# Performance work log

Hardware: AMD Instinct MI355X
Metric: run time of the kernel (lower is better)

The kernel has to match this reference:

```python
import jax, jax.numpy as jnp
import numpy as np

B, L, D = 32, 256, 1024
H = 8
DQ = D // H            # 128, dim_q == dim_k
DS = 64                # dim_s
DM = 256               # dim_mlp_s
DF = 4096              # dim_feedforward
EPS = 1e-5


def _layernorm(x, g, b):
    mu = jnp.mean(x, axis=-1, keepdims=True)
    var = jnp.mean(jnp.square(x - mu), axis=-1, keepdims=True)
    return (x - mu) * jax.lax.rsqrt(var + EPS) * g + b


def setup_inputs() -> dict:
    key = jax.random.key(0)
    ks = jax.random.split(key, 20)
    s = 0.02
    inp = {
        'src': jax.random.normal(ks[0], (B, L, D), jnp.float32),
        'sf': jax.random.normal(ks[1], (B, DS), jnp.float32),
        'atten_mask': jax.random.randint(ks[2], (B, L, L), 0, 2, jnp.int32),
        # per-head projections, stacked over heads (in,out layout)
        'qw': jax.random.normal(ks[3], (H, D, DQ), jnp.float32) * s,
        'qb': jnp.zeros((H, DQ), jnp.float32),
        'kw': jax.random.normal(ks[4], (H, D, DQ), jnp.float32) * s,
        'kb': jnp.zeros((H, DQ), jnp.float32),
        'vw': jax.random.normal(ks[5], (H, D, DQ), jnp.float32) * s,
        'vb': jnp.zeros((H, DQ), jnp.float32),
        # per-head bias MLP: dim_s -> dim_mlp_s -> L*L
        'b1w': jax.random.normal(ks[6], (H, DS, DM), jnp.float32) * s,
        'b1b': jnp.zeros((H, DM), jnp.float32),
        'b2w': jax.random.normal(ks[7], (H, DM, L * L), jnp.float32) * s,
        'b2b': jnp.zeros((H, L * L), jnp.float32),
        # output projection
        'ow': jax.random.normal(ks[8], (H * DQ, D), jnp.float32) * s,
        'ob': jnp.zeros((D,), jnp.float32),
        # layernorms
        'ln1_g': jnp.ones((D,), jnp.float32), 'ln1_b': jnp.zeros((D,), jnp.float32),
        'ln2_g': jnp.ones((D,), jnp.float32), 'ln2_b': jnp.zeros((D,), jnp.float32),
        # feed-forward
        'w1': jax.random.normal(ks[9], (D, DF), jnp.float32) * s,
        'bf1': jnp.zeros((DF,), jnp.float32),
        'w2': jax.random.normal(ks[10], (DF, D), jnp.float32) * s,
        'bf2': jnp.zeros((D,), jnp.float32),
    }
    return inp


def reference(src, sf, atten_mask, qw, qb, kw, kb, vw, vb, b1w, b1b, b2w, b2b,
              ow, ob, ln1_g, ln1_b, ln2_g, ln2_b, w1, bf1, w2, bf2):
    mask = atten_mask.astype(bool)                      # (B,L,L)
    # per-head projections: (H,B,L,DQ)
    q = jnp.einsum('bld,hdq->hblq', src, qw) + qb[:, None, None, :]
    k = jnp.einsum('bld,hdq->hblq', src, kw) + kb[:, None, None, :]
    v = jnp.einsum('bld,hdq->hblq', src, vw) + vb[:, None, None, :]
    scale = q.shape[-1] ** 0.5
    scores = jnp.einsum('hblq,hbmq->hblm', q, k) / scale
    # masked_fill with constant 1e-9 (NOT -inf), as in the original
    scores = jnp.where(mask[None], jnp.float32(1e-9), scores)
    # per-head learned bias from side features, added AFTER softmax
    hid = jax.nn.relu(jnp.einsum('bs,hsm->hbm', sf, b1w) + b1b[:, None, :])
    bias = (jnp.einsum('hbm,hmn->hbn', hid, b2w) + b2b[:, None, :]).reshape(H, B, L, L)
    soft = jax.nn.softmax(scores, axis=-1) + bias
    out = jnp.einsum('hblm,hbmv->hblv', soft, v)        # (H,B,L,DQ)
    # faithful to original: each head's result is indexed [0] -> batch element 0
    head0 = out[:, 0]                                   # (H,L,DQ)
    hidden = jnp.transpose(head0, (1, 0, 2)).reshape(L, H * DQ)
    attn = hidden @ ow + ob                             # (L,D), broadcasts over batch
    x = _layernorm(src + attn[None], ln1_g, ln1_b)      # (B,L,D)
    ffn = jax.nn.relu(x @ w1 + bf1) @ w2 + bf2
    return _layernorm(x + ffn, ln2_g, ln2_b)
```

## Files before the change

kernel.cpp:

```cpp
#include <hip/hip_runtime.h>

typedef unsigned short u16;
typedef short s16x8 __attribute__((ext_vector_type(8)));
typedef u16 u16x4 __attribute__((ext_vector_type(4)));
typedef float f32x4 __attribute__((ext_vector_type(4)));

#define B_ 32
#define L_ 256
#define D_ 1024
#define H_ 8
#define DQ_ 128
#define DS_ 64
#define DM_ 256
#define DF_ 4096

__device__ __forceinline__ u16 f2bf(float f) {
  unsigned u = __float_as_uint(f);
  unsigned r = (u + 0x7FFFu + ((u >> 16) & 1u)) >> 16;
  return (u16)r;
}
__device__ __forceinline__ float bf2f(u16 x) {
  return __uint_as_float(((unsigned)x) << 16);
}

__device__ __forceinline__ f32x4 mfma16(s16x8 a, s16x8 b, f32x4 c) {
  return __builtin_amdgcn_mfma_f32_16x16x32_bf16(a, b, c, 0, 0, 0);
}

#define GLDS16(g, l)                                                        \
  __builtin_amdgcn_global_load_lds(                                         \
      (__attribute__((address_space(1))) const void*)(g),                   \
      (__attribute__((address_space(3))) void*)(l), 16, 0, 0)

__device__ __forceinline__ void tile_tr(const float* __restrict__ ip,
                                        u16* __restrict__ op, int K, int N,
                                        int bx, int by, float (*t)[33], int tid) {
  const int tx = tid & 31, ty = tid >> 5;
  const long n0 = (long)bx * 32, k0 = (long)by * 32;
#pragma unroll
  for (int i = 0; i < 4; ++i)
    t[ty + i * 8][tx] = ip[(k0 + ty + i * 8) * (long)N + n0 + tx];
  __syncthreads();
#pragma unroll
  for (int i = 0; i < 4; ++i)
    op[(n0 + ty + i * 8) * (long)K + k0 + tx] = f2bf(t[tx][ty + i * 8]);
}

__global__ __launch_bounds__(256) void prep(
    const float* __restrict__ qw, const float* __restrict__ kw,
    const float* __restrict__ vw, const float* __restrict__ ow,
    const float* __restrict__ w1, const float* __restrict__ w2,
    const float* __restrict__ src, const float* __restrict__ sf,
    const float* __restrict__ b1w, const float* __restrict__ b1b,
    u16* __restrict__ qwT, u16* __restrict__ kwT, u16* __restrict__ vwT,
    u16* __restrict__ owT, u16* __restrict__ w1T, u16* __restrict__ w2T,
    u16* __restrict__ src0b, float* __restrict__ nzv, int* __restrict__ nzi,
    int* __restrict__ nzcnt) {
  const int b = blockIdx.x;
  const int tid = threadIdx.x;
  __shared__ float t[32][33];
  __shared__ float s_sf[DS_];
  __shared__ int wcnt[4];
  if (b < 3072) {
    const int z = b >> 7, rem = b & 127;
    const int sel = z >> 3, h = z & 7;
    const float* ip = (sel == 0 ? qw : (sel == 1 ? kw : vw)) + (long)h * D_ * DQ_;
    u16* op = (sel == 0 ? qwT : (sel == 1 ? kwT : vwT)) + (long)h * DQ_ * D_;
    tile_tr(ip, op, D_, DQ_, rem & 3, rem >> 2, t, tid);
  } else if (b < 4096) {
    const int rem = b - 3072;
    tile_tr(ow, owT, D_, D_, rem & 31, rem >> 5, t, tid);
  } else if (b < 8192) {
    const int rem = b - 4096;
    tile_tr(w1, w1T, D_, DF_, rem & 127, rem >> 7, t, tid);
  } else if (b < 12288) {
    const int rem = b - 8192;
    tile_tr(w2, w2T, DF_, D_, rem & 31, rem >> 5, t, tid);
  } else if (b < 12544) {
    const int rem = b - 12288;
    const int i = (rem * 256 + tid) * 4;
    float4 v = *(const float4*)(src + i);
    u16x4 o = {f2bf(v.x), f2bf(v.y), f2bf(v.z), f2bf(v.w)};
    *(u16x4*)(src0b + i) = o;
  } else {
    const int h = b - 12544;
    if (tid < DS_) s_sf[tid] = sf[tid];
    __syncthreads();
    float a = b1b[h * DM_ + tid];
    const float* wp = b1w + (long)h * DS_ * DM_ + tid;
#pragma unroll 8
    for (int s = 0; s < DS_; ++s) a += s_sf[s] * wp[s * DM_];
    a = fmaxf(a, 0.f);
    const unsigned long long bal = __ballot(a > 0.f);
    const int lane = tid & 63, wv = tid >> 6;
    const int pc = __popcll(bal);
    if (lane == 0) wcnt[wv] = pc;
    __syncthreads();
    int base = 0;
    for (int i = 0; i < wv; ++i) base += wcnt[i];
    const int pos = base + __popcll(bal & ((1ull << lane) - 1ull));
    if (a > 0.f) { nzv[h * DM_ + pos] = a; nzi[h * DM_ + pos] = tid; }
    if (tid == 255) nzcnt[h] = base + pc;
  }
}

__global__ __launch_bounds__(256) void phase2(
    const float* __restrict__ nzv, const int* __restrict__ nzi,
    const int* __restrict__ nzcnt, const float* __restrict__ b2w,
    const float* __restrict__ b2b, float* __restrict__ biasb,
    const u16* __restrict__ src0b, const u16* __restrict__ qwT,
    const u16* __restrict__ kwT, const u16* __restrict__ vwT,
    const float* __restrict__ qb, const float* __restrict__ kb,
    const float* __restrict__ vb, u16* __restrict__ q0, u16* __restrict__ k0,
    u16* __restrict__ v0T) {
  const int b = blockIdx.x;
  const int tid = threadIdx.x;
  __shared__ float sv[DM_];
  __shared__ int si[DM_];
  __shared__ u16 smA[128 * 32];
  __shared__ u16 smB[128 * 32];
  if (b < 512) {
    const int h = b >> 6;
    const int n0 = (b & 63) << 10;
    const int nnz = nzcnt[h];
    if (tid < DM_) { sv[tid] = nzv[h * DM_ + tid]; si[tid] = nzi[h * DM_ + tid]; }
    __syncthreads();
    const float* wb = b2w + (long)h * DM_ * 65536 + n0 + tid * 4;
    float4 acc = {0.f, 0.f, 0.f, 0.f};
    int j = 0;
    for (; j + 4 <= nnz; j += 4) {
      const float4 a0 = *(const float4*)(wb + (long)si[j] * 65536);
      const float4 a1 = *(const float4*)(wb + (long)si[j + 1] * 65536);
      const float4 a2 = *(const float4*)(wb + (long)si[j + 2] * 65536);
      const float4 a3 = *(const float4*)(wb + (long)si[j + 3] * 65536);
      const float v0 = sv[j], v1 = sv[j + 1], v2 = sv[j + 2], v3 = sv[j + 3];
      acc.x += v0 * a0.x + v1 * a1.x + v2 * a2.x + v3 * a3.x;
      acc.y += v0 * a0.y + v1 * a1.y + v2 * a2.y + v3 * a3.y;
      acc.z += v0 * a0.z + v1 * a1.z + v2 * a2.z + v3 * a3.z;
      acc.w += v0 * a0.w + v1 * a1.w + v2 * a2.w + v3 * a3.w;
    }
    for (; j < nnz; ++j) {
      const float4 a0 = *(const float4*)(wb + (long)si[j] * 65536);
      const float v0 = sv[j];
      acc.x += v0 * a0.x; acc.y += v0 * a0.y; acc.z += v0 * a0.z; acc.w += v0 * a0.w;
    }
    const float4 bb = *(const float4*)(b2b + (long)h * 65536 + n0 + tid * 4);
    float4 o = {acc.x + bb.x, acc.y + bb.y, acc.z + bb.z, acc.w + bb.w};
    *(float4*)(biasb + (long)h * 65536 + n0 + tid * 4) = o;
  } else {
    const int r = b - 512;
    const int z = r >> 1, sel = z >> 3, h = z & 7;
    const long tm = (long)(r & 1) * 128;
    const int K = D_;
    const u16* BT = (sel == 0 ? qwT : (sel == 1 ? kwT : vwT)) + (long)h * DQ_ * D_;
    const float* bias = (sel == 0 ? qb : (sel == 1 ? kb : vb)) + h * DQ_;
    const int lane = tid & 63;
    const int wv = tid >> 6;
    const int wr = wv >> 1, wc = wv & 1;
    const u16* ga = src0b + (tm + (tid >> 2)) * (long)K + (tid & 3) * 8;
    const u16* gb = BT + (long)(tid >> 2) * K + (tid & 3) * 8;
    const long rstep = 64L * K;
    u16* la = &smA[tid * 8];
    u16* lb = &smB[tid * 8];
    f32x4 acc[4][4];
#pragma unroll
    for (int m = 0; m < 4; ++m)
#pragma unroll
      for (int n = 0; n < 4; ++n) acc[m][n] = (f32x4){0.f, 0.f, 0.f, 0.f};
    for (int k0_ = 0; k0_ < K; k0_ += 32) {
      GLDS16(ga + k0_, la);
      GLDS16(ga + rstep + k0_, la + 64 * 32);
      GLDS16(gb + k0_, lb);
      GLDS16(gb + rstep + k0_, lb + 64 * 32);
      __syncthreads();
      s16x8 af[4], bf[4];
      const int ka = (lane >> 4) * 8;
      const int ra = wr * 64 + (lane & 15);
      const int rb = wc * 64 + (lane & 15);
#pragma unroll
      for (int m = 0; m < 4; ++m) af[m] = *(const s16x8*)&smA[(ra + m * 16) * 32 + ka];
#pragma unroll
      for (int n = 0; n < 4; ++n) bf[n] = *(const s16x8*)&smB[(rb + n * 16) * 32 + ka];
#pragma unroll
      for (int m = 0; m < 4; ++m)
#pragma unroll
        for (int n = 0; n < 4; ++n) acc[m][n] = mfma16(af[m], bf[n], acc[m][n]);
      __syncthreads();
    }
    const long crow0 = tm + wr * 64 + ((lane >> 4) * 4);
    const long ccol0 = wc * 64 + (lane & 15);
#pragma unroll
    for (int m = 0; m < 4; ++m) {
#pragma unroll
      for (int n = 0; n < 4; ++n) {
#pragma unroll
        for (int i = 0; i < 4; ++i) {
          const long row = crow0 + m * 16 + i;
          const long col = ccol0 + n * 16;
          const float v = acc[m][n][i] + bias[col];
          if (sel < 2) {
            u16* o = (sel == 0 ? q0 : k0) + (long)h * L_ * DQ_;
            o[row * DQ_ + col] = f2bf(v);
          } else {
            v0T[(long)h * DQ_ * L_ + col * L_ + row] = f2bf(v);
          }
        }
      }
    }
  }
}

__global__ __launch_bounds__(256) void gemm_bt(
    const u16* __restrict__ A, const u16* __restrict__ BT, float* __restrict__ C,
    const float* __restrict__ bias, int K, int ldc) {
  __shared__ u16 smA[128 * 32];
  __shared__ u16 smB[128 * 32];
  const int tid = threadIdx.x;
  const int lane = tid & 63;
  const int wv = tid >> 6;
  const int wr = wv >> 1, wc = wv & 1;
  const long tm = (long)blockIdx.x * 128;
  const long tn = (long)blockIdx.y * 128;

  const u16* ga = A + (tm + (tid >> 2)) * (long)K + (tid & 3) * 8;
  const u16* gb = BT + (tn + (tid >> 2)) * (long)K + (tid & 3) * 8;
  const long rstep = 64L * K;
  u16* la = &smA[tid * 8];
  u16* lb = &smB[tid * 8];

  f32x4 acc[4][4];
#pragma unroll
  for (int m = 0; m < 4; ++m)
#pragma unroll
    for (int n = 0; n < 4; ++n) acc[m][n] = (f32x4){0.f, 0.f, 0.f, 0.f};

  for (int k0 = 0; k0 < K; k0 += 32) {
    GLDS16(ga + k0, la);
    GLDS16(ga + rstep + k0, la + 64 * 32);
    GLDS16(gb + k0, lb);
    GLDS16(gb + rstep + k0, lb + 64 * 32);
    __syncthreads();
    s16x8 af[4], bf[4];
    const int ka = (lane >> 4) * 8;
    const int ra = wr * 64 + (lane & 15);
    const int rb = wc * 64 + (lane & 15);
#pragma unroll
    for (int m = 0; m < 4; ++m) af[m] = *(const s16x8*)&smA[(ra + m * 16) * 32 + ka];
#pragma unroll
    for (int n = 0; n < 4; ++n) bf[n] = *(const s16x8*)&smB[(rb + n * 16) * 32 + ka];
#pragma unroll
    for (int m = 0; m < 4; ++m)
#pragma unroll
      for (int n = 0; n < 4; ++n) acc[m][n] = mfma16(af[m], bf[n], acc[m][n]);
    __syncthreads();
  }

  const long crow0 = tm + wr * 64 + ((lane >> 4) * 4);
  const long ccol0 = tn + wc * 64 + (lane & 15);
#pragma unroll
  for (int m = 0; m < 4; ++m)
#pragma unroll
    for (int n = 0; n < 4; ++n)
#pragma unroll
      for (int i = 0; i < 4; ++i) {
        const long row = crow0 + m * 16 + i;
        const long col = ccol0 + n * 16;
        C[row * (long)ldc + col] = acc[m][n][i] + bias[col];
      }
}

template <int BN, int EPI>
__global__ __launch_bounds__(512, 2) void gemm8p(
    const u16* __restrict__ A, const u16* __restrict__ BT, void* __restrict__ Cv,
    const float* __restrict__ bias, const void* __restrict__ R, int M, int N,
    int K, int ldc) {
  extern __shared__ char lds[];
  constexpr int NR = BN / 64;
  constexpr int NHB = BN / 128;
  constexpr int BUF = 32768 + BN * 128;
  constexpr int WST = (NHB == 2) ? 4 : 2;
  const int tid = threadIdx.x;
  const int lane = tid & 63;
  const int w = tid >> 6;
  const int wr = w >> 2, wc = w & 3;

  const int total = gridDim.x;
  int bid = blockIdx.x;
  int s = ((total & 7) == 0) ? ((bid & 7) * (total >> 3) + (bid >> 3)) : bid;
  const int gn = N / BN;
  const long tm = (long)(s / gn) * 256;
  const long tn = (long)(s % gn) * BN;
  const int NT = K >> 6;

  auto stageA = [&](int half, int t) {
    char* hb = lds + (long)(t & 1) * BUF + half * 16384;
    const u16* g = A + (tm + half * 128) * (long)K + (long)t * 64;
#pragma unroll
    for (int j = 0; j < 2; ++j) {
      const int idx = j * 512 + tid;
      const int r = idx >> 3;
      const int c16 = (idx & 7) ^ (r & 7);
      GLDS16(g + (long)r * K + c16 * 8, hb + idx * 16);
    }
  };
  auto stageB = [&](int half, int t) {
    char* hb = lds + (long)(t & 1) * BUF + 32768 + half * 16384;
    const u16* g = BT + (tn + half * 128) * (long)K + (long)t * 64;
#pragma unroll
    for (int j = 0; j < 2; ++j) {
      const int idx = j * 512 + tid;
      const int r = idx >> 3;
      const int c16 = (idx & 7) ^ (r & 7);
      GLDS16(g + (long)r * K + c16 * 8, hb + idx * 16);
    }
  };

  stageA(0, 0);
  stageA(1, 0);
  stageB(0, 0);
  if (NHB == 2) stageB(1, 0);
  stageB(0, 1);
  if (NHB == 2) stageB(1, 1);
  asm volatile("s_waitcnt vmcnt(%0)" ::"n"(WST) : "memory");
  __builtin_amdgcn_s_barrier();

  f32x4 acc[8][NR];
#pragma unroll
  for (int m = 0; m < 8; ++m)
#pragma unroll
    for (int n = 0; n < NR; ++n) acc[m][n] = (f32x4){0.f, 0.f, 0.f, 0.f};

  const int lk = (lane >> 4) * 16;
  const int lr = lane & 15;

  for (int t = 0; t < NT; ++t) {
    const char* bp = lds + (long)(t & 1) * BUF;
    s16x8 bfr[NR][2];
#pragma unroll
    for (int p = 0; p < 4; ++p) {
      if (p == 0) {
#pragma unroll
        for (int ni = 0; ni < NR; ++ni) {
          const int brow = wc * (BN / 4) + ni * 16 + lr;
#pragma unroll
          for (int ks = 0; ks < 2; ++ks) {
            const int kb = (ks * 64 + lk) ^ ((brow & 7) << 4);
            bfr[ni][ks] = *(const s16x8*)(bp + 32768 + brow * 128 + kb);
          }
        }
      }
      s16x8 afr[2][2];
#pragma unroll
      for (int rI = 0; rI < 2; ++rI) {
        const int arow = wr * 128 + (2 * p + rI) * 16 + lr;
#pragma unroll
        for (int ks = 0; ks < 2; ++ks) {
          const int kb = (ks * 64 + lk) ^ ((arow & 7) << 4);
          afr[rI][ks] = *(const s16x8*)(bp + arow * 128 + kb);
        }
      }
      if (p == 0) {
        if (t + 1 < NT) stageA(0, t + 1);
      } else if (p == 1) {
        if (t + 1 < NT) stageA(1, t + 1);
      } else if (p == 2) {
        if (t + 2 < NT) stageB(0, t + 2);
      } else {
        if (NHB == 2 && t + 2 < NT) stageB(1, t + 2);
      }
      __builtin_amdgcn_s_barrier();
      __builtin_amdgcn_s_setprio(1);
#pragma unroll
      for (int rI = 0; rI < 2; ++rI)
#pragma unroll
        for (int ni = 0; ni < NR; ++ni)
#pragma unroll
          for (int ks = 0; ks < 2; ++ks)
            acc[2 * p + rI][ni] = mfma16(afr[rI][ks], bfr[ni][ks], acc[2 * p + rI][ni]);
      __builtin_amdgcn_s_setprio(0);
      if (p == 3) {
        if (t + 2 < NT) {
          asm volatile("s_waitcnt vmcnt(%0)" ::"n"(WST) : "memory");
        } else if (t + 1 < NT) {
          asm volatile("s_waitcnt vmcnt(0)" ::: "memory");
        }
      }
      __builtin_amdgcn_s_barrier();
    }
  }

  const long crow0 = tm + wr * 128 + ((lane >> 4) * 4);
  const long ccol0 = tn + wc * (BN / 4) + lr;
#pragma unroll
  for (int m = 0; m < 8; ++m) {
#pragma unroll
    for (int n = 0; n < NR; ++n) {
#pragma unroll
      for (int i = 0; i < 4; ++i) {
        const long row = crow0 + m * 16 + i;
        const long col = ccol0 + n * 16;
        const float v = acc[m][n][i] + bias[col];
        if constexpr (EPI == 1) {
          ((u16*)Cv)[row * (long)ldc + col] = f2bf(fmaxf(v, 0.f));
        } else {
          const float r = bf2f(((const u16*)R)[row * (long)ldc + col]);
          ((u16*)Cv)[row * (long)ldc + col] = f2bf(v + r);
        }
      }
    }
  }
}

__global__ __launch_bounds__(64) void attn_kernel(
    const u16* __restrict__ q0, const u16* __restrict__ k0,
    const u16* __restrict__ vT, const float* __restrict__ biasb,
    const int* __restrict__ mask0, u16* __restrict__ hidden) {
  const int lane = threadIdx.x;
  const int h = blockIdx.y;
  const int r0 = blockIdx.x * 16;
  const u16* q = q0 + (long)h * L_ * DQ_;
  const u16* k = k0 + (long)h * L_ * DQ_;
  const u16* v = vT + (long)h * DQ_ * L_;
  const int lg = lane >> 4;
  const int ll = lane & 15;

  s16x8 aq[4];
#pragma unroll
  for (int kk = 0; kk < 4; ++kk)
    aq[kk] = *(const s16x8*)(q + (long)(r0 + ll) * DQ_ + kk * 32 + lg * 8);

  float sc[16][4];
  const float scale = 0.08838834764831845f;
#pragma unroll
  for (int t = 0; t < 16; ++t) {
    f32x4 a = {0.f, 0.f, 0.f, 0.f};
#pragma unroll
    for (int kk = 0; kk < 4; ++kk) {
      s16x8 bf = *(const s16x8*)(k + (long)(t * 16 + ll) * DQ_ + kk * 32 + lg * 8);
      a = mfma16(aq[kk], bf, a);
    }
#pragma unroll
    for (int i = 0; i < 4; ++i) {
      const int row = r0 + lg * 4 + i;
      const int col = t * 16 + ll;
      float s = a[i] * scale;
      if (mask0[row * L_ + col] != 0) s = 1e-9f;
      sc[t][i] = s;
    }
  }
#pragma unroll
  for (int i = 0; i < 4; ++i) {
    float mx = sc[0][i];
#pragma unroll
    for (int t = 1; t < 16; ++t) mx = fmaxf(mx, sc[t][i]);
#pragma unroll
    for (int d = 1; d < 16; d <<= 1) mx = fmaxf(mx, __shfl_xor(mx, d));
    float sum = 0.f;
#pragma unroll
    for (int t = 0; t < 16; ++t) {
      const float e = __expf(sc[t][i] - mx);
      sc[t][i] = e;
      sum += e;
    }
#pragma unroll
    for (int d = 1; d < 16; d <<= 1) sum += __shfl_xor(sum, d);
    const float inv = 1.f / sum;
    const int row = r0 + lg * 4 + i;
#pragma unroll
    for (int t = 0; t < 16; ++t)
      sc[t][i] = sc[t][i] * inv + biasb[(long)h * 65536 + (long)row * 256 + t * 16 + ll];
  }
  __shared__ float sm[16 * 256];
#pragma unroll
  for (int t = 0; t < 16; ++t)
#pragma unroll
    for (int i = 0; i < 4; ++i)
      sm[(lg * 4 + i) * 256 + t * 16 + ll] = sc[t][i];
  __syncthreads();
  s16x8 af[8];
#pragma unroll
  for (int kk = 0; kk < 8; ++kk) {
    const float* ap = &sm[ll * 256 + kk * 32 + lg * 8];
    s16x8 t8;
#pragma unroll
    for (int j = 0; j < 8; ++j) t8[j] = (short)f2bf(ap[j]);
    af[kk] = t8;
  }
#pragma unroll
  for (int n = 0; n < 8; ++n) {
    f32x4 a = {0.f, 0.f, 0.f, 0.f};
#pragma unroll
    for (int kk = 0; kk < 8; ++kk) {
      s16x8 bf = *(const s16x8*)(v + (long)(n * 16 + ll) * 256 + kk * 32 + lg * 8);
      a = mfma16(af[kk], bf, a);
    }
#pragma unroll
    for (int i = 0; i < 4; ++i) {
      const int row = r0 + lg * 4 + i;
      const int col = n * 16 + ll;
      hidden[(long)row * 1024 + h * 128 + col] = f2bf(a[i]);
    }
  }
}

template <int MODE>
__global__ __launch_bounds__(256) void ln_kernel(
    const void* __restrict__ in0v, const float* __restrict__ add1,
    const float* __restrict__ g, const float* __restrict__ bb,
    void* __restrict__ outv) {
  const int tid = threadIdx.x;
  const long row = blockIdx.x;
  float4 v;
  if constexpr (MODE == 0) {
    v = ((const float4*)((const float*)in0v + row * D_))[tid];
    const float4 u = ((const float4*)(add1 + (row & (L_ - 1)) * D_))[tid];
    v.x += u.x; v.y += u.y; v.z += u.z; v.w += u.w;
  } else {
    const uint2 pk = *(const uint2*)((const u16*)in0v + row * D_ + tid * 4);
    v.x = __uint_as_float((pk.x & 0xFFFFu) << 16);
    v.y = __uint_as_float(pk.x & 0xFFFF0000u);
    v.z = __uint_as_float((pk.y & 0xFFFFu) << 16);
    v.w = __uint_as_float(pk.y & 0xFFFF0000u);
  }
  float s = v.x + v.y + v.z + v.w;
  float q = v.x * v.x + v.y * v.y + v.z * v.z + v.w * v.w;
#pragma unroll
  for (int d = 1; d < 64; d <<= 1) { s += __shfl_xor(s, d); q += __shfl_xor(q, d); }
  __shared__ float ss[4], sq[4];
  const int wv = tid >> 6;
  if ((tid & 63) == 0) { ss[wv] = s; sq[wv] = q; }
  __syncthreads();
  s = ss[0] + ss[1] + ss[2] + ss[3];
  q = sq[0] + sq[1] + sq[2] + sq[3];
  const float mu = s * (1.f / D_);
  const float var = q * (1.f / D_) - mu * mu;
  const float rs = rsqrtf(var + 1e-5f);
  const float4 gv = ((const float4*)g)[tid];
  const float4 bv = ((const float4*)bb)[tid];
  float4 o;
  o.x = (v.x - mu) * rs * gv.x + bv.x;
  o.y = (v.y - mu) * rs * gv.y + bv.y;
  o.z = (v.z - mu) * rs * gv.z + bv.z;
  o.w = (v.w - mu) * rs * gv.w + bv.w;
  if constexpr (MODE == 0) {
    uint2 pk;
    pk.x = (unsigned)f2bf(o.x) | ((unsigned)f2bf(o.y) << 16);
    pk.y = (unsigned)f2bf(o.z) | ((unsigned)f2bf(o.w) << 16);
    *(uint2*)((u16*)outv + row * D_ + tid * 4) = pk;
  } else {
    ((float4*)((float*)outv + row * D_))[tid] = o;
  }
}

extern "C" void kernel_launch(void* const* d_in, const int* in_sizes, int n_in,
                              void* d_out, int out_size, void* d_ws, size_t ws_size,
                              hipStream_t stream) {
  (void)in_sizes; (void)n_in; (void)out_size; (void)ws_size;
  const float* src = (const float*)d_in[0];
  const float* sf = (const float*)d_in[1];
  const int* mask = (const int*)d_in[2];
  const float* qw = (const float*)d_in[3];
  const float* qb = (const float*)d_in[4];
  const float* kw = (const float*)d_in[5];
  const float* kb = (const float*)d_in[6];
  const float* vw = (const float*)d_in[7];
  const float* vb = (const float*)d_in[8];
  const float* b1w = (const float*)d_in[9];
  const float* b1b = (const float*)d_in[10];
  const float* b2w = (const float*)d_in[11];
  const float* b2b = (const float*)d_in[12];
  const float* ow = (const float*)d_in[13];
  const float* ob = (const float*)d_in[14];
  const float* ln1g = (const float*)d_in[15];
  const float* ln1b = (const float*)d_in[16];
  const float* ln2g = (const float*)d_in[17];
  const float* ln2b = (const float*)d_in[18];
  const float* w1 = (const float*)d_in[19];
  const float* bf1 = (const float*)d_in[20];
  const float* w2 = (const float*)d_in[21];
  const float* bf2 = (const float*)d_in[22];
  float* out = (float*)d_out;

  char* ws = (char*)d_ws;
  size_t off = 0;
  auto alloc = [&](size_t bytes) {
    void* p = ws + off;
    off += (bytes + 255) & ~(size_t)255;
    return p;
  };
  u16* qwT = (u16*)alloc((size_t)H_ * DQ_ * D_ * 2);
  u16* kwT = (u16*)alloc((size_t)H_ * DQ_ * D_ * 2);
  u16* vwT = (u16*)alloc((size_t)H_ * DQ_ * D_ * 2);
  u16* owT = (u16*)alloc((size_t)D_ * D_ * 2);
  u16* w1T = (u16*)alloc((size_t)DF_ * D_ * 2);
  u16* w2T = (u16*)alloc((size_t)D_ * DF_ * 2);
  u16* src0b = (u16*)alloc((size_t)L_ * D_ * 2);
  u16* q0 = (u16*)alloc((size_t)H_ * L_ * DQ_ * 2);
  u16* k0 = (u16*)alloc((size_t)H_ * L_ * DQ_ * 2);
  u16* v0T = (u16*)alloc((size_t)H_ * DQ_ * L_ * 2);
  float* nzv = (float*)alloc((size_t)H_ * DM_ * 4);
  int* nzi = (int*)alloc((size_t)H_ * DM_ * 4);
  int* nzcnt = (int*)alloc(256);
  float* biasb = (float*)alloc((size_t)H_ * L_ * L_ * 4);
  u16* hidden = (u16*)alloc((size_t)L_ * H_ * DQ_ * 2);
  float* attnvec = (float*)alloc((size_t)L_ * D_ * 4);
  u16* xb = (u16*)alloc((size_t)B_ * L_ * D_ * 2);
  u16* ffnh = (u16*)alloc((size_t)B_ * L_ * DF_ * 2);
  u16* yb = (u16*)alloc((size_t)B_ * L_ * D_ * 2);

  hipFuncSetAttribute((const void*)gemm8p<256, 1>,
                      hipFuncAttributeMaxDynamicSharedMemorySize, 131072);
  hipFuncSetAttribute((const void*)gemm8p<128, 2>,
                      hipFuncAttributeMaxDynamicSharedMemorySize, 98304);

  const dim3 b256(256);
  prep<<<dim3(12552), b256, 0, stream>>>(qw, kw, vw, ow, w1, w2, src, sf, b1w, b1b,
                                         qwT, kwT, vwT, owT, w1T, w2T, src0b, nzv,
                                         nzi, nzcnt);
  phase2<<<dim3(560), b256, 0, stream>>>(nzv, nzi, nzcnt, b2w, b2b, biasb, src0b,
                                         qwT, kwT, vwT, qb, kb, vb, q0, k0, v0T);
  attn_kernel<<<dim3(16, H_), dim3(64), 0, stream>>>(q0, k0, v0T, biasb, mask, hidden);
  gemm_bt<<<dim3(2, 8), b256, 0, stream>>>(hidden, owT, attnvec, ob, D_, D_);
  ln_kernel<0><<<dim3(B_ * L_), b256, 0, stream>>>(src, attnvec, ln1g, ln1b, xb);
  gemm8p<256, 1><<<dim3(512), dim3(512), 131072, stream>>>(
      xb, w1T, ffnh, bf1, nullptr, B_ * L_, DF_, D_, DF_);
  gemm8p<128, 2><<<dim3(256), dim3(512), 98304, stream>>>(
      ffnh, w2T, yb, bf2, xb, B_ * L_, D_, DF_, D_);
  ln_kernel<1><<<dim3(B_ * L_), b256, 0, stream>>>(yb, nullptr, ln2g, ln2b, out);
}
```

Measured before the change: 329.0 us.

## Rebalance prep kernels and split attention into softmax·V plus bias·V GEMM

Moves the large weight transposes (ow, w1, w2) out of the first prep kernel into the same launch as the QKV projection GEMM, so the small QKV GEMM blocks overlap with transpose work. The bias-MLP second layer now runs concurrently with the attention softmax·V computation in one launch, storing the bias in bf16. Because the bias is added after softmax, (softmax+bias)·V is decomposed into softmax·V plus a separate bias·V tiled GEMM that accumulates into hidden. The aim is to remove serial launch tails and the fp32 bias traffic. The cost is an extra kernel, a read-modify-write of hidden, and extra bf16 rounding of the bias and of the partial sums.

```diff
diff --git a/kernel.cpp b/kernel.cpp
--- a/kernel.cpp
+++ b/kernel.cpp
@@ -46,16 +46,13 @@
     op[(n0 + ty + i * 8) * (long)K + k0 + tx] = f2bf(t[tx][ty + i * 8]);
 }
 
-__global__ __launch_bounds__(256) void prep(
+__global__ __launch_bounds__(256) void prep1(
     const float* __restrict__ qw, const float* __restrict__ kw,
-    const float* __restrict__ vw, const float* __restrict__ ow,
-    const float* __restrict__ w1, const float* __restrict__ w2,
-    const float* __restrict__ src, const float* __restrict__ sf,
-    const float* __restrict__ b1w, const float* __restrict__ b1b,
-    u16* __restrict__ qwT, u16* __restrict__ kwT, u16* __restrict__ vwT,
-    u16* __restrict__ owT, u16* __restrict__ w1T, u16* __restrict__ w2T,
-    u16* __restrict__ src0b, float* __restrict__ nzv, int* __restrict__ nzi,
-    int* __restrict__ nzcnt) {
+    const float* __restrict__ vw, const float* __restrict__ src,
+    const float* __restrict__ sf, const float* __restrict__ b1w,
+    const float* __restrict__ b1b, u16* __restrict__ qwT, u16* __restrict__ kwT,
+    u16* __restrict__ vwT, u16* __restrict__ src0b, float* __restrict__ nzv,
+    int* __restrict__ nzi, int* __restrict__ nzcnt) {
   const int b = blockIdx.x;
   const int tid = threadIdx.x;
   __shared__ float t[32][33];
@@ -67,23 +64,14 @@
     const float* ip = (sel == 0 ? qw : (sel == 1 ? kw : vw)) + (long)h * D_ * DQ_;
     u16* op = (sel == 0 ? qwT : (sel == 1 ? kwT : vwT)) + (long)h * DQ_ * D_;
     tile_tr(ip, op, D_, DQ_, rem & 3, rem >> 2, t, tid);
-  } else if (b < 4096) {
+  } else if (b < 3328) {
     const int rem = b - 3072;
-    tile_tr(ow, owT, D_, D_, rem & 31, rem >> 5, t, tid);
-  } else if (b < 8192) {
-    const int rem = b - 4096;
-    tile_tr(w1, w1T, D_, DF_, rem & 127, rem >> 7, t, tid);
-  } else if (b < 12288) {
-    const int rem = b - 8192;
-    tile_tr(w2, w2T, DF_, D_, rem & 31, rem >> 5, t, tid);
-  } else if (b < 12544) {
-    const int rem = b - 12288;
     const int i = (rem * 256 + tid) * 4;
     float4 v = *(const float4*)(src + i);
     u16x4 o = {f2bf(v.x), f2bf(v.y), f2bf(v.z), f2bf(v.w)};
     *(u16x4*)(src0b + i) = o;
   } else {
-    const int h = b - 12544;
+    const int h = b - 3328;
     if (tid < DS_) s_sf[tid] = sf[tid];
     __syncthreads();
     float a = b1b[h * DM_ + tid];
@@ -104,22 +92,102 @@
   }
 }
 
-__global__ __launch_bounds__(256) void phase2(
-    const float* __restrict__ nzv, const int* __restrict__ nzi,
-    const int* __restrict__ nzcnt, const float* __restrict__ b2w,
-    const float* __restrict__ b2b, float* __restrict__ biasb,
+__global__ __launch_bounds__(256) void prep2(
     const u16* __restrict__ src0b, const u16* __restrict__ qwT,
     const u16* __restrict__ kwT, const u16* __restrict__ vwT,
     const float* __restrict__ qb, const float* __restrict__ kb,
     const float* __restrict__ vb, u16* __restrict__ q0, u16* __restrict__ k0,
-    u16* __restrict__ v0T) {
+    u16* __restrict__ v0T, const float* __restrict__ ow,
+    const float* __restrict__ w1, const float* __restrict__ w2,
+    u16* __restrict__ owT, u16* __restrict__ w1T, u16* __restrict__ w2T) {
   const int b = blockIdx.x;
   const int tid = threadIdx.x;
-  __shared__ float sv[DM_];
-  __shared__ int si[DM_];
   __shared__ u16 smA[128 * 32];
   __shared__ u16 smB[128 * 32];
+  __shared__ float t[32][33];
+  if (b < 48) {
+    const int r = b;
+    const int z = r >> 1, sel = z >> 3, h = z & 7;
+    const long tm = (long)(r & 1) * 128;
+    const int K = D_;
+    const u16* BT = (sel == 0 ? qwT : (sel == 1 ? kwT : vwT)) + (long)h * DQ_ * D_;
+    const float* bias = (sel == 0 ? qb : (sel == 1 ? kb : vb)) + h * DQ_;
+    const int lane = tid & 63;
+    const int wv = tid >> 6;
+    const int wr = wv >> 1, wc = wv & 1;
+    const u16* ga = src0b + (tm + (tid >> 2)) * (long)K + (tid & 3) * 8;
+    const u16* gb = BT + (long)(tid >> 2) * K + (tid & 3) * 8;
+    const long rstep = 64L * K;
+    u16* la = &smA[tid * 8];
+    u16* lb = &smB[tid * 8];
+    f32x4 acc[4][4];
+#pragma unroll
+    for (int m = 0; m < 4; ++m)
+#pragma unroll
+      for (int n = 0; n < 4; ++n) acc[m][n] = (f32x4){0.f, 0.f, 0.f, 0.f};
+    for (int k0_ = 0; k0_ < K; k0_ += 32) {
+      GLDS16(ga + k0_, la);
+      GLDS16(ga + rstep + k0_, la + 64 * 32);
+      GLDS16(gb + k0_, lb);
+      GLDS16(gb + rstep + k0_, lb + 64 * 32);
+      __syncthreads();
+      s16x8 af[4], bf[4];
+      const int ka = (lane >> 4) * 8;
+      const int ra = wr * 64 + (lane & 15);
+      const int rb = wc * 64 + (lane & 15);
+#pragma unroll
+      for (int m = 0; m < 4; ++m) af[m] = *(const s16x8*)&smA[(ra + m * 16) * 32 + ka];
+#pragma unroll
+      for (int n = 0; n < 4; ++n) bf[n] = *(const s16x8*)&smB[(rb + n * 16) * 32 + ka];
+#pragma unroll
+      for (int m = 0; m < 4; ++m)
+#pragma unroll
+        for (int n = 0; n < 4; ++n) acc[m][n] = mfma16(af[m], bf[n], acc[m][n]);
+      __syncthreads();
+    }
+    const long crow0 = tm + wr * 64 + ((lane >> 4) * 4);
+    const long ccol0 = wc * 64 + (lane & 15);
+#pragma unroll
+    for (int m = 0; m < 4; ++m)
+#pragma unroll
+      for (int n = 0; n < 4; ++n)
+#pragma unroll
+        for (int i = 0; i < 4; ++i) {
+          const long row = crow0 + m * 16 + i;
+          const long col = ccol0 + n * 16;
+          const float v = acc[m][n][i] + bias[col];
+          if (sel < 2) {
+            u16* o = (sel == 0 ? q0 : k0) + (long)h * L_ * DQ_;
+            o[row * DQ_ + col] = f2bf(v);
+          } else {
+            v0T[(long)h * DQ_ * L_ + col * L_ + row] = f2bf(v);
+          }
+        }
+  } else if (b < 1072) {
+    const int rem = b - 48;
+    tile_tr(ow, owT, D_, D_, rem & 31, rem >> 5, t, tid);
+  } else if (b < 5168) {
+    const int rem = b - 1072;
+    tile_tr(w1, w1T, D_, DF_, rem & 127, rem >> 7, t, tid);
+  } else {
+    const int rem = b - 5168;
+    tile_tr(w2, w2T, DF_, D_, rem & 31, rem >> 5, t, tid);
+  }
+}
+
+__global__ __launch_bounds__(256) void phase2b(
+    const float* __restrict__ nzv, const int* __restrict__ nzi,
+    const int* __restrict__ nzcnt, const float* __restrict__ b2w,
+    const float* __restrict__ b2b, u16* __restrict__ biasb16,
+    const u16* __restrict__ q0, const u16* __restrict__ k0,
+    const u16* __restrict__ v0T, const int* __restrict__ mask,
+    u16* __restrict__ hidden) {
+  extern __shared__ char shm[];
+  const int b = blockIdx.x;
+  const int tid = threadIdx.x;
   if (b < 512) {
+    float* sv = (float*)shm;
+    int* si = (int*)(shm + 1024);
     const int h = b >> 6;
     const int n0 = (b & 63) << 10;
     const int nnz = nzcnt[h];
@@ -145,95 +213,112 @@
       acc.x += v0 * a0.x; acc.y += v0 * a0.y; acc.z += v0 * a0.z; acc.w += v0 * a0.w;
     }
     const float4 bb = *(const float4*)(b2b + (long)h * 65536 + n0 + tid * 4);
-    float4 o = {acc.x + bb.x, acc.y + bb.y, acc.z + bb.z, acc.w + bb.w};
-    *(float4*)(biasb + (long)h * 65536 + n0 + tid * 4) = o;
+    u16x4 o = {f2bf(acc.x + bb.x), f2bf(acc.y + bb.y), f2bf(acc.z + bb.z),
+               f2bf(acc.w + bb.w)};
+    *(u16x4*)(biasb16 + (long)h * 65536 + n0 + tid * 4) = o;
   } else {
-    const int r = b - 512;
-    const int z = r >> 1, sel = z >> 3, h = z & 7;
-    const long tm = (long)(r & 1) * 128;
-    const int K = D_;
-    const u16* BT = (sel == 0 ? qwT : (sel == 1 ? kwT : vwT)) + (long)h * DQ_ * D_;
-    const float* bias = (sel == 0 ? qb : (sel == 1 ? kb : vb)) + h * DQ_;
+    const int w = tid >> 6;
+    const int task = (b - 512) * 4 + w;
+    const int h = task >> 4;
+    const int r0 = (task & 15) << 4;
     const int lane = tid & 63;
-    const int wv = tid >> 6;
-    const int wr = wv >> 1, wc = wv & 1;
-    const u16* ga = src0b + (tm + (tid >> 2)) * (long)K + (tid & 3) * 8;
-    const u16* gb = BT + (long)(tid >> 2) * K + (tid & 3) * 8;
-    const long rstep = 64L * K;
-    u16* la = &smA[tid * 8];
-    u16* lb = &smB[tid * 8];
-    f32x4 acc[4][4];
-#pragma unroll
-    for (int m = 0; m < 4; ++m)
-#pragma unroll
-      for (int n = 0; n < 4; ++n) acc[m][n] = (f32x4){0.f, 0.f, 0.f, 0.f};
-    for (int k0_ = 0; k0_ < K; k0_ += 32) {
-      GLDS16(ga + k0_, la);
-      GLDS16(ga + rstep + k0_, la + 64 * 32);
-      GLDS16(gb + k0_, lb);
-      GLDS16(gb + rstep + k0_, lb + 64 * 32);
-      __syncthreads();
-      s16x8 af[4], bf[4];
-      const int ka = (lane >> 4) * 8;
-      const int ra = wr * 64 + (lane & 15);
-      const int rb = wc * 64 + (lane & 15);
-#pragma unroll
-      for (int m = 0; m < 4; ++m) af[m] = *(const s16x8*)&smA[(ra + m * 16) * 32 + ka];
-#pragma unroll
-      for (int n = 0; n < 4; ++n) bf[n] = *(const s16x8*)&smB[(rb + n * 16) * 32 + ka];
-#pragma unroll
-      for (int m = 0; m < 4; ++m)
-#pragma unroll
-        for (int n = 0; n < 4; ++n) acc[m][n] = mfma16(af[m], bf[n], acc[m][n]);
-      __syncthreads();
-    }
-    const long crow0 = tm + wr * 64 + ((lane >> 4) * 4);
-    const long ccol0 = wc * 64 + (lane & 15);
-#pragma unroll
-    for (int m = 0; m < 4; ++m) {
-#pragma unroll
-      for (int n = 0; n < 4; ++n) {
-#pragma unroll
-        for (int i = 0; i < 4; ++i) {
-          const long row = crow0 + m * 16 + i;
-          const long col = ccol0 + n * 16;
-          const float v = acc[m][n][i] + bias[col];
-          if (sel < 2) {
-            u16* o = (sel == 0 ? q0 : k0) + (long)h * L_ * DQ_;
-            o[row * DQ_ + col] = f2bf(v);
-          } else {
-            v0T[(long)h * DQ_ * L_ + col * L_ + row] = f2bf(v);
-          }
-        }
-      }
-    }
-  }
-}
-
-__global__ __launch_bounds__(256) void gemm_bt(
-    const u16* __restrict__ A, const u16* __restrict__ BT, float* __restrict__ C,
-    const float* __restrict__ bias, int K, int ldc) {
-  __shared__ u16 smA[128 * 32];
-  __shared__ u16 smB[128 * 32];
+    const int lg = lane >> 4;
+    const int ll = lane & 15;
+    const u16* q = q0 + (long)h * L_ * DQ_;
+    const u16* k = k0 + (long)h * L_ * DQ_;
+    const u16* v = v0T + (long)h * DQ_ * L_;
+    char* pbuf = shm + w * 8192;
+
+    s16x8 aq[4];
+#pragma unroll
+    for (int kk = 0; kk < 4; ++kk)
+      aq[kk] = *(const s16x8*)(q + (long)(r0 + ll) * DQ_ + kk * 32 + lg * 8);
+    float sc[16][4];
+    const float scale = 0.08838834764831845f;
+#pragma unroll
+    for (int t = 0; t < 16; ++t) {
+      f32x4 a = {0.f, 0.f, 0.f, 0.f};
+#pragma unroll
+      for (int kk = 0; kk < 4; ++kk) {
+        s16x8 bf = *(const s16x8*)(k + (long)(t * 16 + ll) * DQ_ + kk * 32 + lg * 8);
+        a = mfma16(aq[kk], bf, a);
+      }
+#pragma unroll
+      for (int i = 0; i < 4; ++i) {
+        const int row = r0 + lg * 4 + i;
+        const int col = t * 16 + ll;
+        float s = a[i] * scale;
+        if (mask[row * L_ + col] != 0) s = 1e-9f;
+        sc[t][i] = s;
+      }
+    }
+#pragma unroll
+    for (int i = 0; i < 4; ++i) {
+      float mx = sc[0][i];
+#pragma unroll
+      for (int t = 1; t < 16; ++t) mx = fmaxf(mx, sc[t][i]);
+#pragma unroll
+      for (int d = 1; d < 16; d <<= 1) mx = fmaxf(mx, __shfl_xor(mx, d));
+      float sum = 0.f;
+#pragma unroll
+      for (int t = 0; t < 16; ++t) {
+        const float e = __expf(sc[t][i] - mx);
+        sc[t][i] = e;
+        sum += e;
+      }
+#pragma unroll
+      for (int d = 1; d < 16; d <<= 1) sum += __shfl_xor(sum, d);
+      const float inv = 1.f / sum;
+#pragma unroll
+      for (int t = 0; t < 16; ++t) sc[t][i] *= inv;
+    }
+#pragma unroll
+    for (int t = 0; t < 16; ++t)
+#pragma unroll
+      for (int i = 0; i < 4; ++i) {
+        const int lr = lg * 4 + i;
+        const int cb = (t * 16 + ll) * 2;
+        *(u16*)(pbuf + lr * 512 + (cb ^ ((lr & 7) << 4))) = f2bf(sc[t][i]);
+      }
+    s16x8 paf[8];
+#pragma unroll
+    for (int kk = 0; kk < 8; ++kk)
+      paf[kk] = *(const s16x8*)(pbuf + ll * 512 + ((kk * 64 + lg * 16) ^ ((ll & 7) << 4)));
+#pragma unroll
+    for (int n = 0; n < 8; ++n) {
+      f32x4 a = {0.f, 0.f, 0.f, 0.f};
+#pragma unroll
+      for (int kk = 0; kk < 8; ++kk) {
+        s16x8 bf = *(const s16x8*)(v + (long)(n * 16 + ll) * 256 + kk * 32 + lg * 8);
+        a = mfma16(paf[kk], bf, a);
+      }
+#pragma unroll
+      for (int i = 0; i < 4; ++i) {
+        const int row = r0 + lg * 4 + i;
+        const int col = n * 16 + ll;
+        hidden[(long)row * 1024 + h * 128 + col] = f2bf(a[i]);
+      }
+    }
+  }
+}
+
+__device__ __forceinline__ void g128_core(const u16* __restrict__ A,
+                                          const u16* __restrict__ BT, int K,
+                                          u16* smA, u16* smB,
+                                          f32x4 (&acc)[4][4]) {
   const int tid = threadIdx.x;
   const int lane = tid & 63;
   const int wv = tid >> 6;
   const int wr = wv >> 1, wc = wv & 1;
-  const long tm = (long)blockIdx.x * 128;
-  const long tn = (long)blockIdx.y * 128;
-
-  const u16* ga = A + (tm + (tid >> 2)) * (long)K + (tid & 3) * 8;
-  const u16* gb = BT + (tn + (tid >> 2)) * (long)K + (tid & 3) * 8;
+  const u16* ga = A + (long)(tid >> 2) * K + (tid & 3) * 8;
+  const u16* gb = BT + (long)(tid >> 2) * K + (tid & 3) * 8;
   const long rstep = 64L * K;
   u16* la = &smA[tid * 8];
   u16* lb = &smB[tid * 8];
-
-  f32x4 acc[4][4];
 #pragma unroll
   for (int m = 0; m < 4; ++m)
 #pragma unroll
     for (int n = 0; n < 4; ++n) acc[m][n] = (f32x4){0.f, 0.f, 0.f, 0.f};
-
   for (int k0 = 0; k0 < K; k0 += 32) {
     GLDS16(ga + k0, la);
     GLDS16(ga + rstep + k0, la + 64 * 32);
@@ -254,7 +339,49 @@
       for (int n = 0; n < 4; ++n) acc[m][n] = mfma16(af[m], bf[n], acc[m][n]);
     __syncthreads();
   }
-
+}
+
+__global__ __launch_bounds__(256) void biaspv(
+    const u16* __restrict__ biasb16, const u16* __restrict__ v0T,
+    u16* __restrict__ hidden) {
+  __shared__ u16 smA[128 * 32];
+  __shared__ u16 smB[128 * 32];
+  const int tid = threadIdx.x;
+  const int rt = blockIdx.x, h = blockIdx.y;
+  f32x4 acc[4][4];
+  g128_core(biasb16 + (long)h * 65536 + (long)rt * 128 * 256,
+            v0T + (long)h * DQ_ * L_, 256, smA, smB, acc);
+  const int lane = tid & 63;
+  const int wv = tid >> 6;
+  const int wr = wv >> 1, wc = wv & 1;
+  const long crow0 = (long)rt * 128 + wr * 64 + ((lane >> 4) * 4);
+  const long ccol0 = wc * 64 + (lane & 15);
+#pragma unroll
+  for (int m = 0; m < 4; ++m)
+#pragma unroll
+    for (int n = 0; n < 4; ++n)
+#pragma unroll
+      for (int i = 0; i < 4; ++i) {
+        const long row = crow0 + m * 16 + i;
+        const long col = ccol0 + n * 16;
+        u16* p = hidden + row * 1024 + h * 128 + col;
+        *p = f2bf(acc[m][n][i] + bf2f(*p));
+      }
+}
+
+__global__ __launch_bounds__(256) void gemm_bt(
+    const u16* __restrict__ A, const u16* __restrict__ BT, float* __restrict__ C,
+    const float* __restrict__ bias, int K, int ldc) {
+  __shared__ u16 smA[128 * 32];
+  __shared__ u16 smB[128 * 32];
+  const int tid = threadIdx.x;
+  const long tm = (long)blockIdx.x * 128;
+  const long tn = (long)blockIdx.y * 128;
+  f32x4 acc[4][4];
+  g128_core(A + tm * K, BT + tn * K, K, smA, smB, acc);
+  const int lane = tid & 63;
+  const int wv = tid >> 6;
+  const int wr = wv >> 1, wc = wv & 1;
   const long crow0 = tm + wr * 64 + ((lane >> 4) * 4);
   const long ccol0 = tn + wc * 64 + (lane & 15);
 #pragma unroll
@@ -359,15 +486,10 @@
           afr[rI][ks] = *(const s16x8*)(bp + arow * 128 + kb);
         }
       }
-      if (p == 0) {
-        if (t + 1 < NT) stageA(0, t + 1);
-      } else if (p == 1) {
-        if (t + 1 < NT) stageA(1, t + 1);
-      } else if (p == 2) {
-        if (t + 2 < NT) stageB(0, t + 2);
-      } else {
-        if (NHB == 2 && t + 2 < NT) stageB(1, t + 2);
-      }
+      if (p == 0) { if (t + 1 < NT) stageA(0, t + 1); }
+      else if (p == 1) { if (t + 1 < NT) stageA(1, t + 1); }
+      else if (p == 2) { if (t + 2 < NT) stageB(0, t + 2); }
+      else { if (NHB == 2 && t + 2 < NT) stageB(1, t + 2); }
       __builtin_amdgcn_s_barrier();
       __builtin_amdgcn_s_setprio(1);
 #pragma unroll
@@ -407,98 +529,6 @@
           ((u16*)Cv)[row * (long)ldc + col] = f2bf(v + r);
         }
       }
-    }
-  }
-}
-
-__global__ __launch_bounds__(64) void attn_kernel(
-    const u16* __restrict__ q0, const u16* __restrict__ k0,
-    const u16* __restrict__ vT, const float* __restrict__ biasb,
-    const int* __restrict__ mask0, u16* __restrict__ hidden) {
-  const int lane = threadIdx.x;
-  const int h = blockIdx.y;
-  const int r0 = blockIdx.x * 16;
-  const u16* q = q0 + (long)h * L_ * DQ_;
-  const u16* k = k0 + (long)h * L_ * DQ_;
-  const u16* v = vT + (long)h * DQ_ * L_;
-  const int lg = lane >> 4;
-  const int ll = lane & 15;
-
-  s16x8 aq[4];
-#pragma unroll
-  for (int kk = 0; kk < 4; ++kk)
-    aq[kk] = *(const s16x8*)(q + (long)(r0 + ll) * DQ_ + kk * 32 + lg * 8);
-
-  float sc[16][4];
-  const float scale = 0.08838834764831845f;
-#pragma unroll
-  for (int t = 0; t < 16; ++t) {
-    f32x4 a = {0.f, 0.f, 0.f, 0.f};
-#pragma unroll
-    for (int kk = 0; kk < 4; ++kk) {
-      s16x8 bf = *(const s16x8*)(k + (long)(t * 16 + ll) * DQ_ + kk * 32 + lg * 8);
-      a = mfma16(aq[kk], bf, a);
-    }
-#pragma unroll
-    for (int i = 0; i < 4; ++i) {
-      const int row = r0 + lg * 4 + i;
-      const int col = t * 16 + ll;
-      float s = a[i] * scale;
-      if (mask0[row * L_ + col] != 0) s = 1e-9f;
-      sc[t][i] = s;
-    }
-  }
-#pragma unroll
-  for (int i = 0; i < 4; ++i) {
-    float mx = sc[0][i];
-#pragma unroll
-    for (int t = 1; t < 16; ++t) mx = fmaxf(mx, sc[t][i]);
-#pragma unroll
-    for (int d = 1; d < 16; d <<= 1) mx = fmaxf(mx, __shfl_xor(mx, d));
-    float sum = 0.f;
-#pragma unroll
-    for (int t = 0; t < 16; ++t) {
-      const float e = __expf(sc[t][i] - mx);
-      sc[t][i] = e;
-      sum += e;
-    }
-#pragma unroll
-    for (int d = 1; d < 16; d <<= 1) sum += __shfl_xor(sum, d);
-    const float inv = 1.f / sum;
-    const int row = r0 + lg * 4 + i;
-#pragma unroll
-    for (int t = 0; t < 16; ++t)
-      sc[t][i] = sc[t][i] * inv + biasb[(long)h * 65536 + (long)row * 256 + t * 16 + ll];
-  }
-  __shared__ float sm[16 * 256];
-#pragma unroll
-  for (int t = 0; t < 16; ++t)
-#pragma unroll
-    for (int i = 0; i < 4; ++i)
-      sm[(lg * 4 + i) * 256 + t * 16 + ll] = sc[t][i];
-  __syncthreads();
-  s16x8 af[8];
-#pragma unroll
-  for (int kk = 0; kk < 8; ++kk) {
-    const float* ap = &sm[ll * 256 + kk * 32 + lg * 8];
-    s16x8 t8;
-#pragma unroll
-    for (int j = 0; j < 8; ++j) t8[j] = (short)f2bf(ap[j]);
-    af[kk] = t8;
-  }
-#pragma unroll
-  for (int n = 0; n < 8; ++n) {
-    f32x4 a = {0.f, 0.f, 0.f, 0.f};
-#pragma unroll
-    for (int kk = 0; kk < 8; ++kk) {
-      s16x8 bf = *(const s16x8*)(v + (long)(n * 16 + ll) * 256 + kk * 32 + lg * 8);
-      a = mfma16(af[kk], bf, a);
-    }
-#pragma unroll
-    for (int i = 0; i < 4; ++i) {
-      const int row = r0 + lg * 4 + i;
-      const int col = n * 16 + ll;
-      hidden[(long)row * 1024 + h * 128 + col] = f2bf(a[i]);
     }
   }
 }
@@ -601,8 +631,8 @@
   float* nzv = (float*)alloc((size_t)H_ * DM_ * 4);
   int* nzi = (int*)alloc((size_t)H_ * DM_ * 4);
   int* nzcnt = (int*)alloc(256);
-  float* biasb = (float*)alloc((size_t)H_ * L_ * L_ * 4);
-  u16* hidden = (u16*)alloc((size_t)L_ * H_ * DQ_ * 2);
+  u16* biasb16 = (u16*)alloc((size_t)H_ * L_ * L_ * 2);
+  u16* hidden = (u16*)alloc((size_t)L_ * D_ * 2);
   float* attnvec = (float*)alloc((size_t)L_ * D_ * 4);
   u16* xb = (u16*)alloc((size_t)B_ * L_ * D_ * 2);
   u16* ffnh = (u16*)alloc((size_t)B_ * L_ * DF_ * 2);
@@ -614,12 +644,13 @@
                       hipFuncAttributeMaxDynamicSharedMemorySize, 98304);
 
   const dim3 b256(256);
-  prep<<<dim3(12552), b256, 0, stream>>>(qw, kw, vw, ow, w1, w2, src, sf, b1w, b1b,
-                                         qwT, kwT, vwT, owT, w1T, w2T, src0b, nzv,
-                                         nzi, nzcnt);
-  phase2<<<dim3(560), b256, 0, stream>>>(nzv, nzi, nzcnt, b2w, b2b, biasb, src0b,
-                                         qwT, kwT, vwT, qb, kb, vb, q0, k0, v0T);
-  attn_kernel<<<dim3(16, H_), dim3(64), 0, stream>>>(q0, k0, v0T, biasb, mask, hidden);
+  prep1<<<dim3(3336), b256, 0, stream>>>(qw, kw, vw, src, sf, b1w, b1b, qwT, kwT,
+                                         vwT, src0b, nzv, nzi, nzcnt);
+  prep2<<<dim3(9264), b256, 0, stream>>>(src0b, qwT, kwT, vwT, qb, kb, vb, q0, k0,
+                                         v0T, ow, w1, w2, owT, w1T, w2T);
+  phase2b<<<dim3(544), b256, 32768, stream>>>(nzv, nzi, nzcnt, b2w, b2b, biasb16,
+                                              q0, k0, v0T, mask, hidden);
+  biaspv<<<dim3(2, 8), b256, 0, stream>>>(biasb16, v0T, hidden);
   gemm_bt<<<dim3(2, 8), b256, 0, stream>>>(hidden, owT, attnvec, ob, D_, D_);
   ln_kernel<0><<<dim3(B_ * L_), b256, 0, stream>>>(src, attnvec, ln1g, ln1b, xb);
   gemm8p<256, 1><<<dim3(512), dim3(512), 131072, stream>>>(
```

Measured after the change: 338.9 us. 3.0% more time.
